# Kernel optimization log

Hardware: AMD Instinct MI355X
Metric: run time of the kernel (lower is better)

## Reference

```python
import jax, jax.numpy as jnp
import numpy as np

CAUSAL = True
SOFTMAX_SCALE = 0.125
K_DIFF = 192
MASK_FILL = -1000000.0


def setup_inputs() -> dict:
    key = jax.random.key(0)
    ks = jax.random.split(key, 5)
    shape = (1, 8, 192, 64)  # [batch, n_heads, seq, head_dim]
    return {
        "q": jax.random.normal(ks[0], shape, dtype=jnp.float32),
        "k1": jax.random.normal(ks[1], shape, dtype=jnp.float32),
        "k2": jax.random.normal(ks[2], shape, dtype=jnp.float32),
        "v1": jax.random.normal(ks[3], shape, dtype=jnp.float32),
        "v2": jax.random.normal(ks[4], shape, dtype=jnp.float32),
    }


def reference(q, k1, k2, v1, v2):
    b, n, S, h = q.shape
    # Third-order (trittention) scores.
    score_qk = jnp.einsum("bnth,bnqh->bntq", k2, q)   # [b,n,t,q]
    score_kk = jnp.einsum("bnsh,bnth->bnst", k1, k2)  # [b,n,s,t]
    # score[b,n,s,t,q] = score_kk[b,n,s,t] + score_qk[b,n,t,q]
    score = score_kk[..., None] + score_qk[:, :, None, :, :]
    if CAUSAL:
        # Torch mask (dims named t,s,q over score dims s,t,q):
        # masked where s_score > t_score, t_score > q_score, or t_score - s_score > k_diff
        s_i = jnp.arange(S)[:, None, None]
        t_i = jnp.arange(S)[None, :, None]
        q_i = jnp.arange(S)[None, None, :]
        mask = (s_i > t_i) | (t_i > q_i) | (t_i - s_i > K_DIFF)
        score = jnp.where(mask, MASK_FILL, score)
    pre_softmax_attn_score = score  # [b,n,s,t,q]
    # Rearrange 'b n s t q -> b n q (s t)' and scale.
    flat = jnp.transpose(score, (0, 1, 4, 2, 3)).reshape(b, n, S, S * S) * SOFTMAX_SCALE
    M0 = jnp.max(flat, axis=-1)                       # [b,n,q]
    p = jax.nn.softmax(flat, axis=-1)                  # standard softmax (no +0.01)
    L = jnp.sum(jnp.exp(flat - M0[..., None]), axis=-1) + 0.01
    M = M0 + jnp.log(L)                                # non-standard LSE with +0.01
    # SiLU-gated value combination: v[b,n,s,t,h] = silu(v1[s]) * v2[t]
    v_gated = jax.nn.silu(v1)[:, :, :, None, :] * v2[:, :, None, :, :]
    v_flat = jnp.transpose(v_gated, (0, 1, 4, 2, 3)).reshape(b, n, h, S * S)
    z = jnp.einsum("bnql,bnhl->bnqh", p, v_flat)
    return (z, pre_softmax_attn_score, v_gated, M)
```

## Files before the change

kernel.cpp:

```cpp
#include <hip/hip_runtime.h>
#include <math.h>

#define S 192
#define H 64
#define NH 8
#define SC 0.125f
#define FILLV (-1000000.0f)

__device__ __forceinline__ float wave_max(float v) {
#pragma unroll
  for (int m = 32; m; m >>= 1) v = fmaxf(v, __shfl_xor(v, m));
  return v;
}
__device__ __forceinline__ float wave_sum(float v) {
#pragma unroll
  for (int m = 32; m; m >>= 1) v += __shfl_xor(v, m);
  return v;
}

__global__ __launch_bounds__(256) void prep_kernel(
    const float* __restrict__ q, const float* __restrict__ k1,
    const float* __restrict__ k2, const float* __restrict__ v1,
    float* __restrict__ kk, float* __restrict__ qk,
    float* __restrict__ kkT, float* __restrict__ qkT,
    float* __restrict__ sv1) {
  int b = blockIdx.x;
  if (b < 1152) {
    int p = b / 288, bb = b % 288;
    int n = bb / 36, rem = bb % 36;
    int rt = (rem / 6) * 32;
    int ct = (rem % 6) * 32;
    const float* Abase;
    const float* Bbase;
    float* out;
    if (p == 0)      { Abase = k1; Bbase = k2; out = kk; }
    else if (p == 1) { Abase = k2; Bbase = q;  out = qk; }
    else if (p == 2) { Abase = k2; Bbase = k1; out = kkT; }
    else             { Abase = q;  Bbase = k2; out = qkT; }
    Abase += n * S * H; Bbase += n * S * H; out += n * S * S;

    __shared__ float As[32][65];
    __shared__ float Bs[32][65];
    int tid = threadIdx.x;
    for (int i = tid; i < 32 * 64; i += 256) {
      int r = i >> 6, h = i & 63;
      As[r][h] = Abase[(rt + r) * H + h];
      Bs[r][h] = Bbase[(ct + r) * H + h];
    }
    __syncthreads();
    int r0 = (tid / 16) * 2, c0 = (tid % 16) * 2;
    float a00 = 0.f, a01 = 0.f, a10 = 0.f, a11 = 0.f;
#pragma unroll
    for (int h = 0; h < 64; ++h) {
      float x0 = As[r0][h], x1 = As[r0 + 1][h];
      float y0 = Bs[c0][h], y1 = Bs[c0 + 1][h];
      a00 += x0 * y0; a01 += x0 * y1; a10 += x1 * y0; a11 += x1 * y1;
    }
    out[(rt + r0) * S + ct + c0]         = a00;
    out[(rt + r0) * S + ct + c0 + 1]     = a01;
    out[(rt + r0 + 1) * S + ct + c0]     = a10;
    out[(rt + r0 + 1) * S + ct + c0 + 1] = a11;
  } else {
    int i = (b - 1152) * 256 + threadIdx.x;
    const float4* v4 = (const float4*)v1;
    float4 x = v4[i];
    float4 y;
    y.x = x.x / (1.f + expf(-x.x));
    y.y = x.y / (1.f + expf(-x.y));
    y.z = x.z / (1.f + expf(-x.z));
    y.w = x.w / (1.f + expf(-x.w));
    ((float4*)sv1)[i] = y;
  }
}

__global__ __launch_bounds__(256) void stats_kernel(
    const float* __restrict__ kkT, const float* __restrict__ sv1,
    float* __restrict__ mt, float* __restrict__ St, float* __restrict__ Aw) {
  int n = blockIdx.x / S, t = blockIdx.x % S;
  int tid = threadIdx.x, wv = tid >> 6, lane = tid & 63;
  __shared__ float w[S];
  __shared__ float red[4];
  __shared__ float part[4][H];
  const float* kkr = kkT + n * S * S + t * S;

  float lm = -3.4e38f;
  for (int s = tid; s <= t; s += 256) lm = fmaxf(lm, SC * kkr[s]);
  lm = wave_max(lm);
  if (lane == 0) red[wv] = lm;
  __syncthreads();
  float m = fmaxf(fmaxf(red[0], red[1]), fmaxf(red[2], red[3]));

  float ls = 0.f;
  for (int s = tid; s <= t; s += 256) {
    float e = expf(SC * kkr[s] - m);
    w[s] = e;
    ls += e;
  }
  ls = wave_sum(ls);
  __syncthreads();
  if (lane == 0) red[wv] = ls;
  __syncthreads();
  float Ssum = red[0] + red[1] + red[2] + red[3];
  if (tid == 0) { mt[n * S + t] = m; St[n * S + t] = Ssum; }

  const float* sh = sv1 + n * S * H + lane;
  float acc = 0.f;
  for (int s = wv; s <= t; s += 4) acc += w[s] * sh[s * H];
  part[wv][lane] = acc;
  __syncthreads();
  if (wv == 0)
    Aw[(n * S + t) * H + lane] = part[0][lane] + part[1][lane] + part[2][lane] + part[3][lane];
}

__global__ __launch_bounds__(256) void out_kernel(
    const float* __restrict__ qkT, const float* __restrict__ v2,
    const float* __restrict__ mt, const float* __restrict__ St,
    const float* __restrict__ Aw,
    float* __restrict__ z, float* __restrict__ Mout) {
  int n = blockIdx.x / S, qq = blockIdx.x % S;
  int tid = threadIdx.x, wv = tid >> 6, lane = tid & 63;
  __shared__ float e[S];
  __shared__ float red[4];
  __shared__ float part[4][H];
  const float* qkr = qkT + n * S * S + qq * S;
  const float* mtp = mt + n * S;
  const float* Stp = St + n * S;

  float lm = -3.4e38f;
  for (int t = tid; t <= qq; t += 256) lm = fmaxf(lm, SC * qkr[t] + mtp[t]);
  lm = wave_max(lm);
  if (lane == 0) red[wv] = lm;
  __syncthreads();
  float M0 = fmaxf(fmaxf(red[0], red[1]), fmaxf(red[2], red[3]));

  float ls = 0.f;
  for (int t = tid; t <= qq; t += 256) {
    float ev = expf(SC * qkr[t] + mtp[t] - M0);
    e[t] = ev;
    ls += ev * Stp[t];
  }
  ls = wave_sum(ls);
  __syncthreads();
  if (lane == 0) red[wv] = ls;
  __syncthreads();
  float D = red[0] + red[1] + red[2] + red[3];
  if (tid == 0) Mout[n * S + qq] = M0 + logf(D + 0.01f);

  const float* vh = v2 + n * S * H + lane;
  const float* Ah = Aw + n * S * H + lane;
  float acc = 0.f;
  for (int t = wv; t <= qq; t += 4) acc += e[t] * vh[t * H] * Ah[t * H];
  part[wv][lane] = acc;
  __syncthreads();
  if (wv == 0)
    z[(n * S + qq) * H + lane] =
        (part[0][lane] + part[1][lane] + part[2][lane] + part[3][lane]) / D;
}

__global__ __launch_bounds__(384) void stream_kernel(
    const float* __restrict__ kk, const float* __restrict__ qk,
    const float* __restrict__ sv1, const float* __restrict__ v2,
    float* __restrict__ score, float* __restrict__ vg) {
  int b = blockIdx.x;
  int tid = threadIdx.x;
  if (b < 1536) {
    int n = b / S, s = b % S;
    const float* kkr = kk + (n * S + s) * S;
    const float4* qk4 = (const float4*)(qk + n * S * S);
    float4* out4 = (float4*)(score + (size_t)(n * S + s) * S * S);
    int r = tid / 48;
    int j = tid % 48;
    int q0 = 4 * j;
#pragma unroll 4
    for (int tbase = 0; tbase < S; tbase += 8) {
      int t = tbase + r;
      float kv = kkr[t];
      float4 qv = qk4[t * 48 + j];
      bool rowmask = (t < s);
      float4 v;
      v.x = (rowmask || t > q0)     ? FILLV : kv + qv.x;
      v.y = (rowmask || t > q0 + 1) ? FILLV : kv + qv.y;
      v.z = (rowmask || t > q0 + 2) ? FILLV : kv + qv.z;
      v.w = (rowmask || t > q0 + 3) ? FILLV : kv + qv.w;
      out4[t * 48 + j] = v;
    }
  } else {
    int bb = b - 1536;
    int n = bb / S, s = bb % S;
    const float4* a4 = (const float4*)(sv1 + (n * S + s) * H);
    const float4* b4 = (const float4*)(v2 + n * S * H);
    float4* out4 = (float4*)(vg + (size_t)(n * S + s) * S * H);
#pragma unroll
    for (int it = 0; it < 8; ++it) {
      int i = it * 384 + tid;
      int t = i >> 4, j = i & 15;
      float4 a = a4[j];
      float4 bv = b4[t * 16 + j];
      out4[i] = make_float4(a.x * bv.x, a.y * bv.y, a.z * bv.z, a.w * bv.w);
    }
  }
}

extern "C" void kernel_launch(void* const* d_in, const int* in_sizes, int n_in,
                              void* d_out, int out_size, void* d_ws, size_t ws_size,
                              hipStream_t stream) {
  const float* q  = (const float*)d_in[0];
  const float* k1 = (const float*)d_in[1];
  const float* k2 = (const float*)d_in[2];
  const float* v1 = (const float*)d_in[3];
  const float* v2 = (const float*)d_in[4];
  float* out = (float*)d_out;

  float* z     = out;
  float* score = out + 98304;
  float* vg    = out + 98304 + 56623104;
  float* Mout  = out + 98304 + 56623104 + 18874368;

  float* ws   = (float*)d_ws;
  float* kk   = ws;
  float* qk   = ws + 294912;
  float* kkT  = ws + 589824;
  float* qkT  = ws + 884736;
  float* sv1  = ws + 1179648;
  float* mt   = ws + 1277952;
  float* St   = ws + 1279488;
  float* Aw   = ws + 1281024;

  prep_kernel<<<dim3(1248), dim3(256), 0, stream>>>(q, k1, k2, v1, kk, qk, kkT, qkT, sv1);
  stats_kernel<<<dim3(NH * S), dim3(256), 0, stream>>>(kkT, sv1, mt, St, Aw);
  out_kernel<<<dim3(NH * S), dim3(256), 0, stream>>>(qkT, v2, mt, St, Aw, z, Mout);
  stream_kernel<<<dim3(3072), dim3(384), 0, stream>>>(kk, qk, sv1, v2, score, vg);
}
```

Measured before the change: 358.7 us.

## Fuse four launches into two by merging stats into prep and output into stream

Cuts the launch sequence from four kernels to two. The row statistics now compute the k1·k2 scores in place from shared memory, so the transposed kk matrix is no longer needed, and they apply SiLU on the fly. The z and M computation becomes extra blocks inside the streaming kernel, which writes the score and v_gated tensors. This removes two launch gaps and one workspace matmul. In exchange, the first kernel uses a large shared-memory footprint (about 52 KB), which may limit occupancy, and the stats blocks repeat the k1 load for every t.

```diff
diff --git a/kernel.cpp b/kernel.cpp
--- a/kernel.cpp
+++ b/kernel.cpp
@@ -18,50 +18,50 @@
   return v;
 }
 
-__global__ __launch_bounds__(256) void prep_kernel(
+__global__ __launch_bounds__(256) void k1_kernel(
     const float* __restrict__ q, const float* __restrict__ k1,
     const float* __restrict__ k2, const float* __restrict__ v1,
-    float* __restrict__ kk, float* __restrict__ qk,
-    float* __restrict__ kkT, float* __restrict__ qkT,
-    float* __restrict__ sv1) {
+    float* __restrict__ kk, float* __restrict__ qk, float* __restrict__ qkT,
+    float* __restrict__ sv1,
+    float* __restrict__ mt, float* __restrict__ St, float* __restrict__ Aw) {
+  __shared__ float smem[12996];
   int b = blockIdx.x;
-  if (b < 1152) {
+  int tid = threadIdx.x;
+
+  if (b < 864) {
     int p = b / 288, bb = b % 288;
     int n = bb / 36, rem = bb % 36;
-    int rt = (rem / 6) * 32;
-    int ct = (rem % 6) * 32;
-    const float* Abase;
-    const float* Bbase;
+    int rt = (rem / 6) * 32, ct = (rem % 6) * 32;
+    const float *Abase, *Bbase;
     float* out;
     if (p == 0)      { Abase = k1; Bbase = k2; out = kk; }
     else if (p == 1) { Abase = k2; Bbase = q;  out = qk; }
-    else if (p == 2) { Abase = k2; Bbase = k1; out = kkT; }
     else             { Abase = q;  Bbase = k2; out = qkT; }
     Abase += n * S * H; Bbase += n * S * H; out += n * S * S;
 
-    __shared__ float As[32][65];
-    __shared__ float Bs[32][65];
-    int tid = threadIdx.x;
+    float* As = smem;
+    float* Bs = smem + 2080;
     for (int i = tid; i < 32 * 64; i += 256) {
       int r = i >> 6, h = i & 63;
-      As[r][h] = Abase[(rt + r) * H + h];
-      Bs[r][h] = Bbase[(ct + r) * H + h];
+      As[r * 65 + h] = Abase[(rt + r) * H + h];
+      Bs[r * 65 + h] = Bbase[(ct + r) * H + h];
     }
     __syncthreads();
     int r0 = (tid / 16) * 2, c0 = (tid % 16) * 2;
     float a00 = 0.f, a01 = 0.f, a10 = 0.f, a11 = 0.f;
 #pragma unroll
     for (int h = 0; h < 64; ++h) {
-      float x0 = As[r0][h], x1 = As[r0 + 1][h];
-      float y0 = Bs[c0][h], y1 = Bs[c0 + 1][h];
+      float x0 = As[r0 * 65 + h], x1 = As[(r0 + 1) * 65 + h];
+      float y0 = Bs[c0 * 65 + h], y1 = Bs[(c0 + 1) * 65 + h];
       a00 += x0 * y0; a01 += x0 * y1; a10 += x1 * y0; a11 += x1 * y1;
     }
     out[(rt + r0) * S + ct + c0]         = a00;
     out[(rt + r0) * S + ct + c0 + 1]     = a01;
     out[(rt + r0 + 1) * S + ct + c0]     = a10;
     out[(rt + r0 + 1) * S + ct + c0 + 1] = a11;
-  } else {
-    int i = (b - 1152) * 256 + threadIdx.x;
+
+  } else if (b < 960) {
+    int i = (b - 864) * 256 + tid;
     const float4* v4 = (const float4*)v1;
     float4 x = v4[i];
     float4 y;
@@ -70,99 +70,82 @@
     y.z = x.z / (1.f + expf(-x.z));
     y.w = x.w / (1.f + expf(-x.w));
     ((float4*)sv1)[i] = y;
+
+  } else {
+    int idx = b - 960;
+    int n = idx / S, t = idx % S;
+    int wv = tid >> 6, lane = tid & 63;
+    float* k1s  = smem;
+    float* k2t  = smem + 12480;
+    float* w    = smem + 12544;
+    float* red  = smem + 12736;
+    float* part = smem + 12740;
+
+    const float* k1b = k1 + n * S * H;
+    if (tid < 64) k2t[tid] = k2[(n * S + t) * H + tid];
+    int nel = (t + 1) * 64;
+    for (int i = tid; i < nel; i += 256) {
+      int r = i >> 6, h = i & 63;
+      k1s[r * 65 + h] = k1b[i];
+    }
+    __syncthreads();
+
+    if (tid <= t) {
+      float sc = 0.f;
+#pragma unroll
+      for (int h = 0; h < 64; ++h) sc += k1s[tid * 65 + h] * k2t[h];
+      w[tid] = sc;
+    }
+    __syncthreads();
+
+    float lm = -3.4e38f;
+    if (tid <= t) lm = SC * w[tid];
+    lm = wave_max(lm);
+    if (lane == 0) red[wv] = lm;
+    __syncthreads();
+    float m = fmaxf(fmaxf(red[0], red[1]), fmaxf(red[2], red[3]));
+    __syncthreads();
+
+    float ls = 0.f;
+    if (tid <= t) {
+      float e = expf(SC * w[tid] - m);
+      w[tid] = e;
+      ls = e;
+    }
+    ls = wave_sum(ls);
+    if (lane == 0) red[wv] = ls;
+    __syncthreads();
+    float Ssum = red[0] + red[1] + red[2] + red[3];
+    if (tid == 0) { mt[n * S + t] = m; St[n * S + t] = Ssum; }
+
+    const float* v1h = v1 + n * S * H + lane;
+    float acc = 0.f;
+    for (int s = wv; s <= t; s += 4) {
+      float x = v1h[s * H];
+      acc += w[s] * (x / (1.f + expf(-x)));
+    }
+    part[wv * 64 + lane] = acc;
+    __syncthreads();
+    if (wv == 0)
+      Aw[(n * S + t) * H + lane] =
+          part[lane] + part[64 + lane] + part[128 + lane] + part[192 + lane];
   }
 }
 
-__global__ __launch_bounds__(256) void stats_kernel(
-    const float* __restrict__ kkT, const float* __restrict__ sv1,
-    float* __restrict__ mt, float* __restrict__ St, float* __restrict__ Aw) {
-  int n = blockIdx.x / S, t = blockIdx.x % S;
-  int tid = threadIdx.x, wv = tid >> 6, lane = tid & 63;
-  __shared__ float w[S];
-  __shared__ float red[4];
-  __shared__ float part[4][H];
-  const float* kkr = kkT + n * S * S + t * S;
-
-  float lm = -3.4e38f;
-  for (int s = tid; s <= t; s += 256) lm = fmaxf(lm, SC * kkr[s]);
-  lm = wave_max(lm);
-  if (lane == 0) red[wv] = lm;
-  __syncthreads();
-  float m = fmaxf(fmaxf(red[0], red[1]), fmaxf(red[2], red[3]));
-
-  float ls = 0.f;
-  for (int s = tid; s <= t; s += 256) {
-    float e = expf(SC * kkr[s] - m);
-    w[s] = e;
-    ls += e;
-  }
-  ls = wave_sum(ls);
-  __syncthreads();
-  if (lane == 0) red[wv] = ls;
-  __syncthreads();
-  float Ssum = red[0] + red[1] + red[2] + red[3];
-  if (tid == 0) { mt[n * S + t] = m; St[n * S + t] = Ssum; }
-
-  const float* sh = sv1 + n * S * H + lane;
-  float acc = 0.f;
-  for (int s = wv; s <= t; s += 4) acc += w[s] * sh[s * H];
-  part[wv][lane] = acc;
-  __syncthreads();
-  if (wv == 0)
-    Aw[(n * S + t) * H + lane] = part[0][lane] + part[1][lane] + part[2][lane] + part[3][lane];
-}
-
-__global__ __launch_bounds__(256) void out_kernel(
-    const float* __restrict__ qkT, const float* __restrict__ v2,
+__global__ __launch_bounds__(384) void k2_kernel(
+    const float* __restrict__ kk, const float* __restrict__ qk,
+    const float* __restrict__ qkT, const float* __restrict__ sv1,
+    const float* __restrict__ v2,
     const float* __restrict__ mt, const float* __restrict__ St,
     const float* __restrict__ Aw,
+    float* __restrict__ score, float* __restrict__ vg,
     float* __restrict__ z, float* __restrict__ Mout) {
-  int n = blockIdx.x / S, qq = blockIdx.x % S;
-  int tid = threadIdx.x, wv = tid >> 6, lane = tid & 63;
   __shared__ float e[S];
-  __shared__ float red[4];
-  __shared__ float part[4][H];
-  const float* qkr = qkT + n * S * S + qq * S;
-  const float* mtp = mt + n * S;
-  const float* Stp = St + n * S;
-
-  float lm = -3.4e38f;
-  for (int t = tid; t <= qq; t += 256) lm = fmaxf(lm, SC * qkr[t] + mtp[t]);
-  lm = wave_max(lm);
-  if (lane == 0) red[wv] = lm;
-  __syncthreads();
-  float M0 = fmaxf(fmaxf(red[0], red[1]), fmaxf(red[2], red[3]));
-
-  float ls = 0.f;
-  for (int t = tid; t <= qq; t += 256) {
-    float ev = expf(SC * qkr[t] + mtp[t] - M0);
-    e[t] = ev;
-    ls += ev * Stp[t];
-  }
-  ls = wave_sum(ls);
-  __syncthreads();
-  if (lane == 0) red[wv] = ls;
-  __syncthreads();
-  float D = red[0] + red[1] + red[2] + red[3];
-  if (tid == 0) Mout[n * S + qq] = M0 + logf(D + 0.01f);
-
-  const float* vh = v2 + n * S * H + lane;
-  const float* Ah = Aw + n * S * H + lane;
-  float acc = 0.f;
-  for (int t = wv; t <= qq; t += 4) acc += e[t] * vh[t * H] * Ah[t * H];
-  part[wv][lane] = acc;
-  __syncthreads();
-  if (wv == 0)
-    z[(n * S + qq) * H + lane] =
-        (part[0][lane] + part[1][lane] + part[2][lane] + part[3][lane]) / D;
-}
-
-__global__ __launch_bounds__(384) void stream_kernel(
-    const float* __restrict__ kk, const float* __restrict__ qk,
-    const float* __restrict__ sv1, const float* __restrict__ v2,
-    float* __restrict__ score, float* __restrict__ vg) {
+  __shared__ float red[6];
+  __shared__ float part[6 * 64];
   int b = blockIdx.x;
   int tid = threadIdx.x;
+
   if (b < 1536) {
     int n = b / S, s = b % S;
     const float* kkr = kk + (n * S + s) * S;
@@ -184,7 +167,8 @@
       v.w = (rowmask || t > q0 + 3) ? FILLV : kv + qv.w;
       out4[t * 48 + j] = v;
     }
-  } else {
+
+  } else if (b < 3072) {
     int bb = b - 1536;
     int n = bb / S, s = bb % S;
     const float4* a4 = (const float4*)(sv1 + (n * S + s) * H);
@@ -197,6 +181,48 @@
       float4 a = a4[j];
       float4 bv = b4[t * 16 + j];
       out4[i] = make_float4(a.x * bv.x, a.y * bv.y, a.z * bv.z, a.w * bv.w);
+    }
+
+  } else {
+    int idx = b - 3072;
+    int n = idx / S, qq = idx % S;
+    int wv = tid >> 6, lane = tid & 63;
+    const float* qkr = qkT + n * S * S + qq * S;
+    const float* mtp = mt + n * S;
+    const float* Stp = St + n * S;
+
+    float lm = -3.4e38f;
+    if (tid <= qq) lm = SC * qkr[tid] + mtp[tid];
+    lm = wave_max(lm);
+    if (lane == 0) red[wv] = lm;
+    __syncthreads();
+    float M0 = red[0];
+#pragma unroll
+    for (int i = 1; i < 6; ++i) M0 = fmaxf(M0, red[i]);
+    __syncthreads();
+
+    float ls = 0.f;
+    if (tid <= qq) {
+      float ev = expf(SC * qkr[tid] + mtp[tid] - M0);
+      e[tid] = ev;
+      ls = ev * Stp[tid];
+    }
+    ls = wave_sum(ls);
+    if (lane == 0) red[wv] = ls;
+    __syncthreads();
+    float D = red[0] + red[1] + red[2] + red[3] + red[4] + red[5];
+    if (tid == 0) Mout[n * S + qq] = M0 + logf(D + 0.01f);
+
+    const float* vh = v2 + n * S * H + lane;
+    const float* Ah = Aw + n * S * H + lane;
+    float acc = 0.f;
+    for (int t = wv; t <= qq; t += 6) acc += e[t] * vh[t * H] * Ah[t * H];
+    part[wv * 64 + lane] = acc;
+    __syncthreads();
+    if (wv == 0) {
+      float zsum = part[lane] + part[64 + lane] + part[128 + lane] +
+                   part[192 + lane] + part[256 + lane] + part[320 + lane];
+      z[(n * S + qq) * H + lane] = zsum / D;
     }
   }
 }
@@ -219,15 +245,14 @@
   float* ws   = (float*)d_ws;
   float* kk   = ws;
   float* qk   = ws + 294912;
-  float* kkT  = ws + 589824;
-  float* qkT  = ws + 884736;
-  float* sv1  = ws + 1179648;
-  float* mt   = ws + 1277952;
-  float* St   = ws + 1279488;
-  float* Aw   = ws + 1281024;
-
-  prep_kernel<<<dim3(1248), dim3(256), 0, stream>>>(q, k1, k2, v1, kk, qk, kkT, qkT, sv1);
-  stats_kernel<<<dim3(NH * S), dim3(256), 0, stream>>>(kkT, sv1, mt, St, Aw);
-  out_kernel<<<dim3(NH * S), dim3(256), 0, stream>>>(qkT, v2, mt, St, Aw, z, Mout);
-  stream_kernel<<<dim3(3072), dim3(384), 0, stream>>>(kk, qk, sv1, v2, score, vg);
-}
+  float* qkT  = ws + 589824;
+  float* sv1  = ws + 884736;
+  float* mt   = ws + 983040;
+  float* St   = ws + 984576;
+  float* Aw   = ws + 986112;
+
+  k1_kernel<<<dim3(2496), dim3(256), 0, stream>>>(q, k1, k2, v1, kk, qk, qkT,
+                                                  sv1, mt, St, Aw);
+  k2_kernel<<<dim3(4608), dim3(384), 0, stream>>>(kk, qk, qkT, sv1, v2, mt, St,
+                                                  Aw, score, vg, z, Mout);
+}
```

New measurement: 366.3 us. 2.1% more time.
